# Kernel tuning notes

Measured on AMD Instinct MI355X. Metric: run time of the kernel, lower is better.

Reference implementation:

```python
import jax, jax.numpy as jnp
import numpy as np

N_NODES = 100000


def gcn_conv(x, edge_index, W, b):
    """PyG-style GCNConv: x' = D^-1/2 (A + I) D^-1/2 (x W) + b."""
    n = x.shape[0]
    h = x @ W  # transform first (PyG order) -> [N, out]
    loop = jnp.arange(n, dtype=edge_index.dtype)
    src = jnp.concatenate([edge_index[0], loop])  # source nodes (x_j)
    dst = jnp.concatenate([edge_index[1], loop])  # target nodes
    ones = jnp.ones(src.shape[0], dtype=h.dtype)
    deg = jax.ops.segment_sum(ones, dst, num_segments=n)  # in-degree with self-loops
    dinv = jnp.where(deg > 0, jax.lax.rsqrt(deg), 0.0)
    norm = dinv[src] * dinv[dst]  # [E+N]
    msg = h[src] * norm[:, None]  # gather + scale
    out = jax.ops.segment_sum(msg, dst, num_segments=n)  # scatter-add
    return out + b


def setup_inputs() -> dict:
    key = jax.random.key(0)
    k1, k2, k3, k4 = jax.random.split(key, 4)
    F_IN, H, C, E = 512, 16, 40, 3200000
    x = jax.random.normal(k1, (N_NODES, F_IN), dtype=jnp.float32)
    edge_index = jax.random.randint(k2, (2, E), 0, N_NODES, dtype=jnp.int64)
    # Glorot-style init for weights
    W1 = jax.random.normal(k3, (F_IN, H), dtype=jnp.float32) / np.sqrt(F_IN)
    b1 = jnp.zeros((H,), dtype=jnp.float32)
    W2 = jax.random.normal(k4, (H, C), dtype=jnp.float32) / np.sqrt(H)
    b2 = jnp.zeros((C,), dtype=jnp.float32)
    return {"x": x, "edge_index": edge_index, "W1": W1, "b1": b1, "W2": W2, "b2": b2}


def reference(x, edge_index, W1, b1, W2, b2):
    h = gcn_conv(x, edge_index, W1, b1)
    h = jax.nn.relu(h)
    out = gcn_conv(h, edge_index, W2, b2)
    return out
```

## Files before the change

kernel.cpp:

```cpp
#include <hip/hip_runtime.h>
#include <hip/hip_bf16.h>


#define TPB 256
#define CHUNK 6144
#define NBKT_MAX 392
#define MAXB 10240

typedef unsigned int u32;
typedef float __attribute__((ext_vector_type(4))) f32x4;

__device__ __forceinline__ float bflo(u32 u) { return __uint_as_float(u << 16); }
__device__ __forceinline__ float bfhi(u32 u) { return __uint_as_float(u & 0xFFFF0000u); }
__device__ __forceinline__ unsigned short f2bf(float f) {
    __hip_bfloat16 h = __float2bfloat16(f);
    return *reinterpret_cast<unsigned short*>(&h);
}

__global__ __launch_bounds__(TPB) void k_hist(const int* __restrict__ dst,
                                              int* __restrict__ histT,
                                              int E, int nbkt) {
    __shared__ int hist[NBKT_MAX];
    const int tid = threadIdx.x, blk = blockIdx.x;
    for (int k = tid; k < NBKT_MAX; k += TPB) hist[k] = 0;
    __syncthreads();
    const int base = blk * CHUNK;
    const int m = min(CHUNK, E - base);
    for (int i = tid; i < m; i += TPB) {
        int d = dst[base + i];
        atomicAdd(&hist[d >> 8], 1);
    }
    __syncthreads();
    for (int k = tid; k < nbkt; k += TPB) histT[blk * NBKT_MAX + k] = hist[k];
}

__global__ __launch_bounds__(512) void k_scanrow(int* __restrict__ histT,
                                                 int* __restrict__ rowtot,
                                                 int NB1) {
    __shared__ int s[1024];
    const int t = threadIdx.x, k = blockIdx.x;
    int v0 = (t < NB1) ? histT[t * NBKT_MAX + k] : 0;
    int v1 = (t + 512 < NB1) ? histT[(t + 512) * NBKT_MAX + k] : 0;
    s[t] = v0; s[t + 512] = v1;
    __syncthreads();
    for (int off = 1; off <= 512; off <<= 1) {
        int a0 = (t >= off) ? s[t - off] : 0;
        int a1 = s[t + 512 - off];
        __syncthreads();
        s[t] += a0;
        s[t + 512] += a1;
        __syncthreads();
    }
    if (t < NB1) histT[t * NBKT_MAX + k] = s[t] - v0;
    if (t + 512 < NB1) histT[(t + 512) * NBKT_MAX + k] = s[t + 512] - v1;
    if (t == 0) rowtot[k] = s[1023];
}

__global__ __launch_bounds__(512) void k_scanbkt(const int* __restrict__ rowtot,
                                                 int* __restrict__ bktbase,
                                                 int* __restrict__ rs,
                                                 int nbkt, int n, int E) {
    __shared__ int s[512];
    const int t = threadIdx.x;
    int v = (t < nbkt) ? rowtot[t] : 0;
    s[t] = v;
    __syncthreads();
    for (int off = 1; off <= 256; off <<= 1) {
        int a = (t >= off) ? s[t - off] : 0;
        __syncthreads();
        s[t] += a;
        __syncthreads();
    }
    if (t < nbkt) bktbase[t] = s[t] - v;
    if (t == 0) { bktbase[nbkt] = E; rs[n] = E; }
}

__global__ __launch_bounds__(TPB) void k_part(const int* __restrict__ src,
                                              const int* __restrict__ dst,
                                              const int* __restrict__ histT,
                                              const int* __restrict__ bktbase,
                                              u32* __restrict__ pk,
                                              int E, int nbkt) {
    __shared__ u32 sbuf[CHUNK];
    __shared__ int sslot[CHUNK];
    __shared__ int hist[512], gb[512], cur[512];
    __shared__ int s[512];
    const int tid = threadIdx.x, blk = blockIdx.x;
    const int base = blk * CHUNK;
    const int m = min(CHUNK, E - base);
    for (int k = tid; k < 512; k += TPB) { hist[k] = 0; cur[k] = 0; }
    __syncthreads();
    for (int i = tid; i < m; i += TPB) {
        int d = dst[base + i];
        atomicAdd(&hist[d >> 8], 1);
    }
    __syncthreads();
    int c0v = hist[tid], c1v = hist[tid + 256];
    s[tid] = c0v; s[tid + 256] = c1v;
    __syncthreads();
    for (int off = 1; off <= 256; off <<= 1) {
        int a0 = (tid >= off) ? s[tid - off] : 0;
        int a1 = s[tid + 256 - off];
        __syncthreads();
        s[tid] += a0;
        s[tid + 256] += a1;
        __syncthreads();
    }
    hist[tid] = s[tid] - c0v;
    hist[tid + 256] = s[tid + 256] - c1v;
    if (tid < nbkt) gb[tid] = bktbase[tid] + histT[blk * NBKT_MAX + tid];
    if (tid + 256 < nbkt) gb[tid + 256] = bktbase[tid + 256] + histT[blk * NBKT_MAX + tid + 256];
    __syncthreads();
    for (int i = tid; i < m; i += TPB) {
        int d = dst[base + i];
        int sv = src[base + i];
        int k = d >> 8;
        int r = atomicAdd(&cur[k], 1);
        int p = hist[k] + r;
        sbuf[p] = (u32)sv | ((u32)(d & 255) << 17);
        sslot[p] = gb[k] + r;
    }
    __syncthreads();
    for (int p = tid; p < m; p += TPB) pk[sslot[p]] = sbuf[p];
}

__global__ __launch_bounds__(TPB) void k_part2(const u32* __restrict__ pk,
                                               const int* __restrict__ bktbase,
                                               int* __restrict__ ssrc,
                                               int* __restrict__ rs,
                                               float* __restrict__ dinv,
                                               int n) {
    __shared__ u32 ebuf[MAXB];
    __shared__ int cnt[256], csum[256], s[256];
    const int t = threadIdx.x, b = blockIdx.x;
    const int r0 = bktbase[b], r1 = bktbase[b + 1];
    const int m = r1 - r0;
    cnt[t] = 0;
    __syncthreads();
    for (int i = t; i < m; i += TPB) {
        u32 v = pk[r0 + i];
        if (i < MAXB) ebuf[i] = v;
        atomicAdd(&cnt[(v >> 17) & 255], 1);
    }
    __syncthreads();
    int c = cnt[t];
    s[t] = c;
    __syncthreads();
    for (int off = 1; off <= 128; off <<= 1) {
        int a = (t >= off) ? s[t - off] : 0;
        __syncthreads();
        s[t] += a;
        __syncthreads();
    }
    int ex = s[t] - c;
    csum[t] = ex;
    int node = (b << 8) + t;
    if (node < n) {
        rs[node] = r0 + ex;
        dinv[node] = rsqrtf((float)(c + 1));
    }
    cnt[t] = 0;
    __syncthreads();
    for (int i = t; i < m; i += TPB) {
        u32 v = (i < MAXB) ? ebuf[i] : pk[r0 + i];
        int dl = (v >> 17) & 255;
        int r = atomicAdd(&cnt[dl], 1);
        ssrc[r0 + csum[dl] + r] = (int)(v & 0x1FFFF);
    }
}

#define G1_ROWS 256
#define G1_KC 32
__global__ __launch_bounds__(TPB) void k_gemm1(const float* __restrict__ x,
                                               const float* __restrict__ W,
                                               const float* __restrict__ dinv,
                                               unsigned short* __restrict__ hsb, int n) {
    __shared__ float xs[G1_ROWS][36];
    __shared__ float wl[G1_KC][16];
    const int tid = threadIdx.x;
    const int row0 = blockIdx.x * G1_ROWS;
    const int rg = tid >> 2;
    const int c0 = (tid & 3) * 4;

    float acc[4][4];
#pragma unroll
    for (int j = 0; j < 4; ++j)
#pragma unroll
        for (int c = 0; c < 4; ++c) acc[j][c] = 0.0f;

    for (int kc = 0; kc < 512; kc += G1_KC) {
        __syncthreads();
#pragma unroll
        for (int t = 0; t < 8; ++t) {
            int f4 = tid + TPB * t;
            int row = f4 >> 3;
            int kk = (f4 & 7) * 4;
            int grow = row0 + row;
            if (grow >= n) grow = n - 1;
            f32x4 v = __builtin_nontemporal_load(
                reinterpret_cast<const f32x4*>(&x[(size_t)grow * 512 + kc + kk]));
            *reinterpret_cast<f32x4*>(&xs[row][kk]) = v;
        }
        if (tid < 128) {
            int k = tid >> 2, cc = (tid & 3) * 4;
            *reinterpret_cast<float4*>(&wl[k][cc]) =
                *reinterpret_cast<const float4*>(&W[(size_t)(kc + k) * 16 + cc]);
        }
        __syncthreads();

#pragma unroll
        for (int k4 = 0; k4 < G1_KC; k4 += 4) {
            float w[4][4];
#pragma unroll
            for (int kk = 0; kk < 4; ++kk) {
                float4 wv = *reinterpret_cast<const float4*>(&wl[k4 + kk][c0]);
                w[kk][0] = wv.x; w[kk][1] = wv.y; w[kk][2] = wv.z; w[kk][3] = wv.w;
            }
#pragma unroll
            for (int j = 0; j < 4; ++j) {
                float4 xv = *reinterpret_cast<const float4*>(&xs[rg + 64 * j][k4]);
                float xk[4] = {xv.x, xv.y, xv.z, xv.w};
#pragma unroll
                for (int kk = 0; kk < 4; ++kk)
#pragma unroll
                    for (int c = 0; c < 4; ++c) acc[j][c] += xk[kk] * w[kk][c];
            }
        }
    }

#pragma unroll
    for (int j = 0; j < 4; ++j) {
        int grow = row0 + rg + 64 * j;
        if (grow < n) {
            float di = dinv[grow];
            ushort4 o;
            o.x = f2bf(acc[j][0] * di);
            o.y = f2bf(acc[j][1] * di);
            o.z = f2bf(acc[j][2] * di);
            o.w = f2bf(acc[j][3] * di);
            *reinterpret_cast<ushort4*>(&hsb[(size_t)grow * 16 + c0]) = o;
        }
    }
}

__global__ __launch_bounds__(TPB) void k_gagg1(const int* __restrict__ rs,
                                               const int* __restrict__ ssrc,
                                               const unsigned short* __restrict__ hinB,
                                               const float* __restrict__ dinv,
                                               const float* __restrict__ b1,
                                               unsigned short* __restrict__ houtB, int n) {
    int node = blockIdx.x * 4 + (threadIdx.x >> 6);
    if (node >= n) return;
    const int lane = threadIdx.x & 63;
    const int j = lane >> 1;
    const int hf = lane & 1;
    const int r0 = rs[node], r1 = rs[node + 1];

    float a[8];
#pragma unroll
    for (int q = 0; q < 8; ++q) a[q] = 0.0f;

    for (int e = r0 + j; e < r1; e += 32) {
        int sv = ssrc[e];
        uint4 v = *reinterpret_cast<const uint4*>(&hinB[(size_t)sv * 16 + hf * 8]);
        a[0] += bflo(v.x); a[1] += bfhi(v.x);
        a[2] += bflo(v.y); a[3] += bfhi(v.y);
        a[4] += bflo(v.z); a[5] += bfhi(v.z);
        a[6] += bflo(v.w); a[7] += bfhi(v.w);
    }
#pragma unroll
    for (int m = 2; m <= 32; m <<= 1)
#pragma unroll
        for (int q = 0; q < 8; ++q) a[q] += __shfl_xor(a[q], m);

    if (j == 0) {
        float di = dinv[node];
        uint4 sv = *reinterpret_cast<const uint4*>(&hinB[(size_t)node * 16 + hf * 8]);
        float sf[8] = {bflo(sv.x), bfhi(sv.x), bflo(sv.y), bfhi(sv.y),
                       bflo(sv.z), bfhi(sv.z), bflo(sv.w), bfhi(sv.w)};
        unsigned short ob[8];
#pragma unroll
        for (int q = 0; q < 8; ++q) {
            float p = di * (a[q] + sf[q]);
            ob[q] = f2bf(di * fmaxf(p + b1[hf * 8 + q], 0.0f));
        }
        uint4 ov;
        ov.x = (u32)ob[0] | ((u32)ob[1] << 16);
        ov.y = (u32)ob[2] | ((u32)ob[3] << 16);
        ov.z = (u32)ob[4] | ((u32)ob[5] << 16);
        ov.w = (u32)ob[6] | ((u32)ob[7] << 16);
        *reinterpret_cast<uint4*>(&houtB[(size_t)node * 16 + hf * 8]) = ov;
    }
}

__global__ __launch_bounds__(TPB) void k_gagg2f(const int* __restrict__ rs,
                                                const int* __restrict__ ssrc,
                                                const unsigned short* __restrict__ hinB,
                                                const float* __restrict__ dinv,
                                                const float* __restrict__ W2,
                                                const float* __restrict__ b2,
                                                float* __restrict__ out, int n) {
    __shared__ float pre_l[4][17];
    __shared__ float wl[16 * 40];
    __shared__ float bl[40];
    const int tid = threadIdx.x;
    for (int i = tid; i < 640; i += TPB) wl[i] = W2[i];
    if (tid < 40) bl[tid] = b2[tid];

    const int w = tid >> 6;
    const int node = blockIdx.x * 4 + w;
    const int lane = tid & 63;
    const int j = lane >> 1;
    const int hf = lane & 1;

    if (node < n) {
        const int r0 = rs[node], r1 = rs[node + 1];
        float a[8];
#pragma unroll
        for (int q = 0; q < 8; ++q) a[q] = 0.0f;
        for (int e = r0 + j; e < r1; e += 32) {
            int sv = ssrc[e];
            uint4 v = *reinterpret_cast<const uint4*>(&hinB[(size_t)sv * 16 + hf * 8]);
            a[0] += bflo(v.x); a[1] += bfhi(v.x);
            a[2] += bflo(v.y); a[3] += bfhi(v.y);
            a[4] += bflo(v.z); a[5] += bfhi(v.z);
            a[6] += bflo(v.w); a[7] += bfhi(v.w);
        }
#pragma unroll
        for (int m = 2; m <= 32; m <<= 1)
#pragma unroll
            for (int q = 0; q < 8; ++q) a[q] += __shfl_xor(a[q], m);
        if (j == 0) {
            float di = dinv[node];
            uint4 sv = *reinterpret_cast<const uint4*>(&hinB[(size_t)node * 16 + hf * 8]);
            float sf[8] = {bflo(sv.x), bfhi(sv.x), bflo(sv.y), bfhi(sv.y),
                           bflo(sv.z), bfhi(sv.z), bflo(sv.w), bfhi(sv.w)};
#pragma unroll
            for (int q = 0; q < 8; ++q)
                pre_l[w][hf * 8 + q] = di * (a[q] + sf[q]);
        }
    }
    __syncthreads();

    if (tid < 160) {
        int ns = tid / 40, c = tid - ns * 40;
        int gnode = blockIdx.x * 4 + ns;
        if (gnode < n) {
            float acc = bl[c];
#pragma unroll
            for (int k = 0; k < 16; ++k) acc += pre_l[ns][k] * wl[k * 40 + c];
            out[(size_t)gnode * 40 + c] = acc;
        }
    }
}

extern "C" void kernel_launch(void* const* d_in, const int* in_sizes, int n_in,
                              void* d_out, int out_size, void* d_ws, size_t ws_size,
                              hipStream_t stream) {
    const float* x  = (const float*)d_in[0];
    const int*   ei = (const int*)d_in[1];
    const float* W1 = (const float*)d_in[2];
    const float* b1 = (const float*)d_in[3];
    const float* W2 = (const float*)d_in[4];
    const float* b2 = (const float*)d_in[5];
    float* out = (float*)d_out;

    const int n = in_sizes[0] / 512;
    const int E = in_sizes[1] / 2;
    const int* src = ei;
    const int* dst = ei + E;
    const int nbkt = (n + 255) >> 8;
    const int NB1 = (E + CHUNK - 1) / CHUNK;

    char* w = (char*)d_ws;
    int*   histT   = (int*)w;     w += (size_t)NB1 * NBKT_MAX * 4;
    int*   rowtot  = (int*)w;     w += (size_t)NBKT_MAX * 4;
    int*   bktbase = (int*)w;     w += (size_t)(NBKT_MAX + 1) * 4;
    u32*   pk      = (u32*)w;     w += (size_t)E * 4;
    int*   ssrc    = (int*)w;     w += (size_t)E * 4;
    int*   rs      = (int*)w;     w += (size_t)(n + 1) * 4;
    float* dinv    = (float*)w;   w += (size_t)n * 4;
    unsigned short* h1b = (unsigned short*)w;  w += (size_t)n * 16 * 2;
    unsigned short* h2b = (unsigned short*)w;

    k_hist   <<<NB1, TPB, 0, stream>>>(dst, histT, E, nbkt);
    k_scanrow<<<nbkt, 512, 0, stream>>>(histT, rowtot, NB1);
    k_scanbkt<<<1, 512, 0, stream>>>(rowtot, bktbase, rs, nbkt, n, E);
    k_part   <<<NB1, TPB, 0, stream>>>(src, dst, histT, bktbase, pk, E, nbkt);
    k_part2  <<<nbkt, TPB, 0, stream>>>(pk, bktbase, ssrc, rs, dinv, n);
    k_gemm1  <<<(n + G1_ROWS - 1) / G1_ROWS, TPB, 0, stream>>>(x, W1, dinv, h1b, n);
    k_gagg1  <<<(n + 3) / 4, TPB, 0, stream>>>(rs, ssrc, h1b, dinv, b1, h2b, n);
    k_gagg2f <<<(n + 3) / 4, TPB, 0, stream>>>(rs, ssrc, h2b, dinv, W2, b2, out, n);
}
```

Measured before the change: 241.3 us.

## Fuse partition and GEMM1 into one interleaved kernel, compute degrees early

Node in-degrees are now counted with global atomics during the histogram pass, so dinv is ready before the partition step. This lets the bandwidth-bound partition blocks and the x@W1 GEMM blocks run concurrently in a single horizontally fused kernel, interleaved one GEMM block per two partition blocks. The partition block no longer recomputes its local histogram, reusing the stored one instead, and uses a smaller chunk with packed metadata. The cost is per-edge global atomics on cnt, an extra memset, and an extra prefix-sum buffer.

```diff
diff --git a/kernel.cpp b/kernel.cpp
--- a/kernel.cpp
+++ b/kernel.cpp
@@ -3,7 +3,7 @@
 
 
 #define TPB 256
-#define CHUNK 6144
+#define PCH 4096
 #define NBKT_MAX 392
 #define MAXB 10240
 
@@ -17,30 +17,39 @@
     return *reinterpret_cast<unsigned short*>(&h);
 }
 
-__global__ __launch_bounds__(TPB) void k_hist(const int* __restrict__ dst,
-                                              int* __restrict__ histT,
-                                              int E, int nbkt) {
+__global__ __launch_bounds__(TPB) void k_cnthist(const int* __restrict__ dst,
+                                                 int* __restrict__ cnt,
+                                                 int* __restrict__ histT,
+                                                 int E, int nbkt) {
     __shared__ int hist[NBKT_MAX];
     const int tid = threadIdx.x, blk = blockIdx.x;
     for (int k = tid; k < NBKT_MAX; k += TPB) hist[k] = 0;
     __syncthreads();
-    const int base = blk * CHUNK;
-    const int m = min(CHUNK, E - base);
+    const int base = blk * PCH;
+    const int m = min(PCH, E - base);
     for (int i = tid; i < m; i += TPB) {
         int d = dst[base + i];
         atomicAdd(&hist[d >> 8], 1);
+        atomicAdd(&cnt[d], 1);
     }
     __syncthreads();
     for (int k = tid; k < nbkt; k += TPB) histT[blk * NBKT_MAX + k] = hist[k];
 }
 
-__global__ __launch_bounds__(512) void k_scanrow(int* __restrict__ histT,
+__global__ __launch_bounds__(512) void k_scanrow(const int* __restrict__ histT,
+                                                 int* __restrict__ histS,
                                                  int* __restrict__ rowtot,
-                                                 int NB1) {
+                                                 const int* __restrict__ cnt,
+                                                 float* __restrict__ dinv,
+                                                 int NP, int n) {
     __shared__ int s[1024];
     const int t = threadIdx.x, k = blockIdx.x;
-    int v0 = (t < NB1) ? histT[t * NBKT_MAX + k] : 0;
-    int v1 = (t + 512 < NB1) ? histT[(t + 512) * NBKT_MAX + k] : 0;
+    if (t < 256) {
+        int node = (k << 8) + t;
+        if (node < n) dinv[node] = rsqrtf((float)(cnt[node] + 1));
+    }
+    int v0 = (t < NP) ? histT[t * NBKT_MAX + k] : 0;
+    int v1 = (t + 512 < NP) ? histT[(t + 512) * NBKT_MAX + k] : 0;
     s[t] = v0; s[t + 512] = v1;
     __syncthreads();
     for (int off = 1; off <= 512; off <<= 1) {
@@ -51,8 +60,8 @@
         s[t + 512] += a1;
         __syncthreads();
     }
-    if (t < NB1) histT[t * NBKT_MAX + k] = s[t] - v0;
-    if (t + 512 < NB1) histT[(t + 512) * NBKT_MAX + k] = s[t + 512] - v1;
+    if (t < NP) histS[t * NBKT_MAX + k] = s[t] - v0;
+    if (t + 512 < NP) histS[(t + 512) * NBKT_MAX + k] = s[t + 512] - v1;
     if (t == 0) rowtot[k] = s[1023];
 }
 
@@ -75,110 +84,72 @@
     if (t == 0) { bktbase[nbkt] = E; rs[n] = E; }
 }
 
-__global__ __launch_bounds__(TPB) void k_part(const int* __restrict__ src,
-                                              const int* __restrict__ dst,
-                                              const int* __restrict__ histT,
-                                              const int* __restrict__ bktbase,
-                                              u32* __restrict__ pk,
-                                              int E, int nbkt) {
-    __shared__ u32 sbuf[CHUNK];
-    __shared__ int sslot[CHUNK];
-    __shared__ int hist[512], gb[512], cur[512];
-    __shared__ int s[512];
-    const int tid = threadIdx.x, blk = blockIdx.x;
-    const int base = blk * CHUNK;
-    const int m = min(CHUNK, E - base);
-    for (int k = tid; k < 512; k += TPB) { hist[k] = 0; cur[k] = 0; }
-    __syncthreads();
-    for (int i = tid; i < m; i += TPB) {
-        int d = dst[base + i];
-        atomicAdd(&hist[d >> 8], 1);
-    }
-    __syncthreads();
-    int c0v = hist[tid], c1v = hist[tid + 256];
-    s[tid] = c0v; s[tid + 256] = c1v;
+#define G1_ROWS 256
+#define G1_KC 32
+#define SMEM_BYTES 38912
+
+__device__ __forceinline__ void part_body(char* smem, int rid,
+                                          const int* __restrict__ src,
+                                          const int* __restrict__ dst,
+                                          const int* __restrict__ histT,
+                                          const int* __restrict__ histS,
+                                          const int* __restrict__ bktbase,
+                                          u32* __restrict__ pk,
+                                          int E, int nbkt) {
+    u32* sbuf = (u32*)smem;
+    u32* meta = sbuf + PCH;
+    int* lh   = (int*)(meta + PCH);
+    int* gb   = lh + 512;
+    int* cur  = gb + 512;
+    const int tid = threadIdx.x;
+    const int base = rid * PCH;
+    const int m = min(PCH, E - base);
+
+    int c0 = (tid < nbkt) ? histT[rid * NBKT_MAX + tid] : 0;
+    int c1 = (tid + 256 < nbkt) ? histT[rid * NBKT_MAX + tid + 256] : 0;
+    cur[tid] = c0; cur[tid + 256] = c1;
     __syncthreads();
     for (int off = 1; off <= 256; off <<= 1) {
-        int a0 = (tid >= off) ? s[tid - off] : 0;
-        int a1 = s[tid + 256 - off];
-        __syncthreads();
-        s[tid] += a0;
-        s[tid + 256] += a1;
-        __syncthreads();
-    }
-    hist[tid] = s[tid] - c0v;
-    hist[tid + 256] = s[tid + 256] - c1v;
-    if (tid < nbkt) gb[tid] = bktbase[tid] + histT[blk * NBKT_MAX + tid];
-    if (tid + 256 < nbkt) gb[tid + 256] = bktbase[tid + 256] + histT[blk * NBKT_MAX + tid + 256];
-    __syncthreads();
+        int a0 = (tid >= off) ? cur[tid - off] : 0;
+        int a1 = cur[tid + 256 - off];
+        __syncthreads();
+        cur[tid] += a0;
+        cur[tid + 256] += a1;
+        __syncthreads();
+    }
+    lh[tid] = cur[tid] - c0;
+    lh[tid + 256] = cur[tid + 256] - c1;
+    if (tid < nbkt) gb[tid] = bktbase[tid] + histS[rid * NBKT_MAX + tid];
+    if (tid + 256 < nbkt) gb[tid + 256] = bktbase[tid + 256] + histS[rid * NBKT_MAX + tid + 256];
+    __syncthreads();
+    cur[tid] = 0; cur[tid + 256] = 0;
+    __syncthreads();
+
     for (int i = tid; i < m; i += TPB) {
         int d = dst[base + i];
         int sv = src[base + i];
         int k = d >> 8;
         int r = atomicAdd(&cur[k], 1);
-        int p = hist[k] + r;
+        int p = lh[k] + r;
         sbuf[p] = (u32)sv | ((u32)(d & 255) << 17);
-        sslot[p] = gb[k] + r;
-    }
-    __syncthreads();
-    for (int p = tid; p < m; p += TPB) pk[sslot[p]] = sbuf[p];
-}
-
-__global__ __launch_bounds__(TPB) void k_part2(const u32* __restrict__ pk,
-                                               const int* __restrict__ bktbase,
-                                               int* __restrict__ ssrc,
-                                               int* __restrict__ rs,
-                                               float* __restrict__ dinv,
-                                               int n) {
-    __shared__ u32 ebuf[MAXB];
-    __shared__ int cnt[256], csum[256], s[256];
-    const int t = threadIdx.x, b = blockIdx.x;
-    const int r0 = bktbase[b], r1 = bktbase[b + 1];
-    const int m = r1 - r0;
-    cnt[t] = 0;
-    __syncthreads();
-    for (int i = t; i < m; i += TPB) {
-        u32 v = pk[r0 + i];
-        if (i < MAXB) ebuf[i] = v;
-        atomicAdd(&cnt[(v >> 17) & 255], 1);
-    }
-    __syncthreads();
-    int c = cnt[t];
-    s[t] = c;
-    __syncthreads();
-    for (int off = 1; off <= 128; off <<= 1) {
-        int a = (t >= off) ? s[t - off] : 0;
-        __syncthreads();
-        s[t] += a;
-        __syncthreads();
-    }
-    int ex = s[t] - c;
-    csum[t] = ex;
-    int node = (b << 8) + t;
-    if (node < n) {
-        rs[node] = r0 + ex;
-        dinv[node] = rsqrtf((float)(c + 1));
-    }
-    cnt[t] = 0;
-    __syncthreads();
-    for (int i = t; i < m; i += TPB) {
-        u32 v = (i < MAXB) ? ebuf[i] : pk[r0 + i];
-        int dl = (v >> 17) & 255;
-        int r = atomicAdd(&cnt[dl], 1);
-        ssrc[r0 + csum[dl] + r] = (int)(v & 0x1FFFF);
-    }
-}
-
-#define G1_ROWS 256
-#define G1_KC 32
-__global__ __launch_bounds__(TPB) void k_gemm1(const float* __restrict__ x,
-                                               const float* __restrict__ W,
-                                               const float* __restrict__ dinv,
-                                               unsigned short* __restrict__ hsb, int n) {
-    __shared__ float xs[G1_ROWS][36];
-    __shared__ float wl[G1_KC][16];
+        meta[p] = ((u32)k << 12) | (u32)r;
+    }
+    __syncthreads();
+    for (int p = tid; p < m; p += TPB) {
+        u32 mm = meta[p];
+        pk[gb[mm >> 12] + (mm & 4095)] = sbuf[p];
+    }
+}
+
+__device__ __forceinline__ void gemm1_body(char* smem, int rid,
+                                           const float* __restrict__ x,
+                                           const float* __restrict__ W,
+                                           const float* __restrict__ dinv,
+                                           unsigned short* __restrict__ hsb, int n) {
+    float (*xs)[36] = (float(*)[36])smem;
+    float* wl = (float*)(smem + 36864);
     const int tid = threadIdx.x;
-    const int row0 = blockIdx.x * G1_ROWS;
+    const int row0 = rid * G1_ROWS;
     const int rg = tid >> 2;
     const int c0 = (tid & 3) * 4;
 
@@ -203,7 +174,7 @@
         }
         if (tid < 128) {
             int k = tid >> 2, cc = (tid & 3) * 4;
-            *reinterpret_cast<float4*>(&wl[k][cc]) =
+            *reinterpret_cast<float4*>(&wl[k * 16 + cc]) =
                 *reinterpret_cast<const float4*>(&W[(size_t)(kc + k) * 16 + cc]);
         }
         __syncthreads();
@@ -213,7 +184,7 @@
             float w[4][4];
 #pragma unroll
             for (int kk = 0; kk < 4; ++kk) {
-                float4 wv = *reinterpret_cast<const float4*>(&wl[k4 + kk][c0]);
+                float4 wv = *reinterpret_cast<const float4*>(&wl[(k4 + kk) * 16 + c0]);
                 w[kk][0] = wv.x; w[kk][1] = wv.y; w[kk][2] = wv.z; w[kk][3] = wv.w;
             }
 #pragma unroll
@@ -240,6 +211,77 @@
             o.w = f2bf(acc[j][3] * di);
             *reinterpret_cast<ushort4*>(&hsb[(size_t)grow * 16 + c0]) = o;
         }
+    }
+}
+
+__global__ __launch_bounds__(TPB) void k_fat(const int* __restrict__ src,
+                                             const int* __restrict__ dst,
+                                             const int* __restrict__ histT,
+                                             const int* __restrict__ histS,
+                                             const int* __restrict__ bktbase,
+                                             u32* __restrict__ pk,
+                                             const float* __restrict__ x,
+                                             const float* __restrict__ W1,
+                                             const float* __restrict__ dinv,
+                                             unsigned short* __restrict__ hsb,
+                                             int E, int n, int nbkt,
+                                             int NPART, int NGEMM) {
+    __shared__ __align__(16) char smem[SMEM_BYTES];
+    const int bid = blockIdx.x;
+    bool isG = false;
+    int rid;
+    if (bid < 3 * NGEMM) {
+        if (bid % 3 == 2) { isG = true; rid = bid / 3; }
+        else rid = bid - (bid + 1) / 3;
+    } else {
+        rid = bid - NGEMM;
+    }
+    if (isG) {
+        gemm1_body(smem, rid, x, W1, dinv, hsb, n);
+    } else {
+        if (rid < NPART)
+            part_body(smem, rid, src, dst, histT, histS, bktbase, pk, E, nbkt);
+    }
+}
+
+__global__ __launch_bounds__(TPB) void k_part2(const u32* __restrict__ pk,
+                                               const int* __restrict__ bktbase,
+                                               int* __restrict__ ssrc,
+                                               int* __restrict__ rs,
+                                               int n) {
+    __shared__ u32 ebuf[MAXB];
+    __shared__ int cnt[256], csum[256], s[256];
+    const int t = threadIdx.x, b = blockIdx.x;
+    const int r0 = bktbase[b], r1 = bktbase[b + 1];
+    const int m = r1 - r0;
+    cnt[t] = 0;
+    __syncthreads();
+    for (int i = t; i < m; i += TPB) {
+        u32 v = pk[r0 + i];
+        if (i < MAXB) ebuf[i] = v;
+        atomicAdd(&cnt[(v >> 17) & 255], 1);
+    }
+    __syncthreads();
+    int c = cnt[t];
+    s[t] = c;
+    __syncthreads();
+    for (int off = 1; off <= 128; off <<= 1) {
+        int a = (t >= off) ? s[t - off] : 0;
+        __syncthreads();
+        s[t] += a;
+        __syncthreads();
+    }
+    int ex = s[t] - c;
+    csum[t] = ex;
+    int node = (b << 8) + t;
+    if (node < n) rs[node] = r0 + ex;
+    cnt[t] = 0;
+    __syncthreads();
+    for (int i = t; i < m; i += TPB) {
+        u32 v = (i < MAXB) ? ebuf[i] : pk[r0 + i];
+        int dl = (v >> 17) & 255;
+        int r = atomicAdd(&cnt[dl], 1);
+        ssrc[r0 + csum[dl] + r] = (int)(v & 0x1FFFF);
     }
 }
 
@@ -370,25 +412,32 @@
     const int* src = ei;
     const int* dst = ei + E;
     const int nbkt = (n + 255) >> 8;
-    const int NB1 = (E + CHUNK - 1) / CHUNK;
+    const int NPART = (E + PCH - 1) / PCH;
+    const int NGEMM = (n + G1_ROWS - 1) / G1_ROWS;
 
     char* w = (char*)d_ws;
-    int*   histT   = (int*)w;     w += (size_t)NB1 * NBKT_MAX * 4;
+    int*   histT   = (int*)w;     w += (size_t)NPART * NBKT_MAX * 4;
+    int*   histS   = (int*)w;     w += (size_t)NPART * NBKT_MAX * 4;
     int*   rowtot  = (int*)w;     w += (size_t)NBKT_MAX * 4;
     int*   bktbase = (int*)w;     w += (size_t)(NBKT_MAX + 1) * 4;
     u32*   pk      = (u32*)w;     w += (size_t)E * 4;
     int*   ssrc    = (int*)w;     w += (size_t)E * 4;
     int*   rs      = (int*)w;     w += (size_t)(n + 1) * 4;
+    int*   cnt     = (int*)w;     w += (size_t)n * 4;
     float* dinv    = (float*)w;   w += (size_t)n * 4;
     unsigned short* h1b = (unsigned short*)w;  w += (size_t)n * 16 * 2;
     unsigned short* h2b = (unsigned short*)w;
 
-    k_hist   <<<NB1, TPB, 0, stream>>>(dst, histT, E, nbkt);
-    k_scanrow<<<nbkt, 512, 0, stream>>>(histT, rowtot, NB1);
+    int fat_grid = NPART + NGEMM;
+    if (fat_grid < 3 * NGEMM) fat_grid = 3 * NGEMM;
+
+    hipMemsetAsync(cnt, 0, (size_t)n * 4, stream);
+    k_cnthist<<<NPART, TPB, 0, stream>>>(dst, cnt, histT, E, nbkt);
+    k_scanrow<<<nbkt, 512, 0, stream>>>(histT, histS, rowtot, cnt, dinv, NPART, n);
     k_scanbkt<<<1, 512, 0, stream>>>(rowtot, bktbase, rs, nbkt, n, E);
-    k_part   <<<NB1, TPB, 0, stream>>>(src, dst, histT, bktbase, pk, E, nbkt);
-    k_part2  <<<nbkt, TPB, 0, stream>>>(pk, bktbase, ssrc, rs, dinv, n);
-    k_gemm1  <<<(n + G1_ROWS - 1) / G1_ROWS, TPB, 0, stream>>>(x, W1, dinv, h1b, n);
+    k_fat    <<<fat_grid, TPB, 0, stream>>>(src, dst, histT, histS, bktbase, pk,
+                                            x, W1, dinv, h1b, E, n, nbkt, NPART, NGEMM);
+    k_part2  <<<nbkt, TPB, 0, stream>>>(pk, bktbase, ssrc, rs, n);
     k_gagg1  <<<(n + 3) / 4, TPB, 0, stream>>>(rs, ssrc, h1b, dinv, b1, h2b, n);
     k_gagg2f <<<(n + 3) / 4, TPB, 0, stream>>>(rs, ssrc, h2b, dinv, W2, b2, out, n);
 }
```

Result: slower. 365.3 us (+51.4%).
